# Kernel optimization log

Measured on AMD Instinct MI355X. Metric: run time of the kernel, lower is better.

Reference implementation:

```python
import jax, jax.numpy as jnp
import numpy as np
import math

B, S, D, H = 4, 2048, 1024, 16
DK = D // H


def setup_inputs() -> dict:
    key = jax.random.key(0)
    ks = jax.random.split(key, 11)
    s = 1.0 / math.sqrt(D)
    inp = {
        "query": jax.random.normal(ks[0], (B, S, D), jnp.float32),
        "key": jax.random.normal(ks[1], (B, S, D), jnp.float32),
        "value": jax.random.normal(ks[2], (B, S, D), jnp.float32),
        # torch nn.Linear params: weight [out,in], bias [out]
        "Wq": jax.random.uniform(ks[3], (D, D), jnp.float32, -s, s),
        "bq": jax.random.uniform(ks[4], (D,), jnp.float32, -s, s),
        "Wk": jax.random.uniform(ks[5], (D, D), jnp.float32, -s, s),
        "bk": jax.random.uniform(ks[6], (D,), jnp.float32, -s, s),
        "Wv": jax.random.uniform(ks[7], (D, D), jnp.float32, -s, s),
        "bv": jax.random.uniform(ks[8], (D,), jnp.float32, -s, s),
        "Wo": jax.random.uniform(ks[9], (D, D), jnp.float32, -s, s),
        "bo": jax.random.uniform(ks[10], (D,), jnp.float32, -s, s),
    }
    return inp


def _split_heads(x):
    # [B,S,D] -> [B,H,S,DK]
    return x.reshape(B, S, H, DK).transpose(0, 2, 1, 3)


def reference(query, key, value, Wq, bq, Wk, bk, Wv, bv, Wo, bo):
    q = _split_heads(query @ Wq.T + bq)
    k = _split_heads(key @ Wk.T + bk)
    v = _split_heads(value @ Wv.T + bv)
    scores = jnp.einsum("bhqd,bhkd->bhqk", q, k) / math.sqrt(DK)
    p = jax.nn.softmax(scores, axis=-1)  # dropout p=0 -> identity
    x = jnp.einsum("bhqk,bhkd->bhqd", p, v)
    x = x.transpose(0, 2, 1, 3).reshape(B, S, D)
    return x @ Wo.T + bo
```

## Files before the change

### kernel.cpp

```cpp
#include <hip/hip_runtime.h>
#include <hip/hip_bf16.h>


typedef __attribute__((ext_vector_type(8))) short bf16x8;
typedef __attribute__((ext_vector_type(4))) float f32x4;

static __device__ __forceinline__ unsigned short f2bf(float f) {
  union { __hip_bfloat16 h; unsigned short u; } cv;
  cv.h = __float2bfloat16(f);
  return cv.u;
}

static __device__ __forceinline__ unsigned int pack2bf(float a, float b) {
  union { __hip_bfloat162 h; unsigned int u; } cv;
  cv.h = __float22bfloat162_rn(float2{a, b});
  return cv.u;
}

static __device__ __forceinline__ void pl32swap(unsigned int& a, unsigned int& b) {
  asm volatile("v_permlane32_swap_b32 %0, %1" : "+v"(a), "+v"(b));
}
static __device__ __forceinline__ void pl16swap(unsigned int& a, unsigned int& b) {
  asm volatile("v_permlane16_swap_b32 %0, %1" : "+v"(a), "+v"(b));
}

static __device__ __forceinline__ void gload_lds16(const void* g, void* l) {
  __builtin_amdgcn_global_load_lds(
      (const __attribute__((address_space(1))) unsigned int*)g,
      (__attribute__((address_space(3))) unsigned int*)l, 16, 0, 0);
}

template<int NJ>
struct CvtJobs { const float* in[NJ]; unsigned short* out[NJ]; int n; };

template<int NJ>
__global__ __launch_bounds__(256) void cvt_batch(CvtJobs<NJ> jobs) {
  const float* __restrict__ in = jobs.in[blockIdx.y];
  unsigned short* __restrict__ out = jobs.out[blockIdx.y];
  int i = (blockIdx.x * 256 + threadIdx.x) * 4;
  if (i + 3 < jobs.n) {
    float4 v = *(const float4*)(in + i);
    ushort4 o;
    o.x = f2bf(v.x); o.y = f2bf(v.y); o.z = f2bf(v.z); o.w = f2bf(v.w);
    *(ushort4*)(out + i) = o;
  }
}

template<int MODE>
__global__ __launch_bounds__(256) void gemm_bt(const unsigned short* __restrict__ A_,
                                               const unsigned short* __restrict__ Bw_,
                                               const float* __restrict__ bias,
                                               const float* __restrict__ bias1,
                                               void* __restrict__ outp,
                                               int M, int N, int K) {
  __shared__ unsigned short As[128 * 32];
  __shared__ unsigned short Bs[128 * 32];
  const int tid = threadIdx.x;
  const int w = tid >> 6, lane = tid & 63;
  const int wr = w >> 1, wc = w & 1;
  const int fr = lane & 15, fg = lane >> 4;

  const unsigned short* A = A_;
  const unsigned short* Bw = Bw_;
  float scale = 1.f;
  unsigned short* out16 = (unsigned short*)outp;
  if (MODE == 4) {
    const int z = blockIdx.z;
    A += (size_t)z * (8192 * 1024);
    Bw += (size_t)z * (1024 * 1024);
    out16 += (size_t)z * (8192 * 1024);
    if (z == 0) scale = 0.18033688011f;
    else bias = bias1;
  }

  int bx, by;
  if (MODE != 2) {
    const int nwg = gridDim.x * gridDim.y;
    const int lin = blockIdx.y * gridDim.x + blockIdx.x;
    const int nb = (lin & 7) * (nwg >> 3) + (lin >> 3);
    bx = nb % gridDim.x; by = nb / gridDim.x;
  } else {
    bx = blockIdx.x; by = blockIdx.y;
  }
  const int m0 = by * 128, n0 = bx * 128;

  f32x4 acc[4][4] = {};
  const int e0 = (w * 2) * 512 + lane * 8;

  for (int kt = 0; kt < K; kt += 32) {
#pragma unroll
    for (int i = 0; i < 2; ++i) {
      const int e = e0 + i * 512;
      const int row = e >> 5, kk = e & 31;
      gload_lds16(A + (size_t)(m0 + row) * K + kt + kk, (void*)(As + e));
      gload_lds16(Bw + (size_t)(n0 + row) * K + kt + kk, (void*)(Bs + e));
    }
    __syncthreads();
    bf16x8 af[4], bfr[4];
#pragma unroll
    for (int m = 0; m < 4; ++m)
      af[m] = *(const bf16x8*)(As + (wr * 64 + m * 16 + fr) * 32 + fg * 8);
#pragma unroll
    for (int n = 0; n < 4; ++n)
      bfr[n] = *(const bf16x8*)(Bs + (wc * 64 + n * 16 + fr) * 32 + fg * 8);
#pragma unroll
    for (int m = 0; m < 4; ++m)
#pragma unroll
      for (int n = 0; n < 4; ++n)
        acc[m][n] = __builtin_amdgcn_mfma_f32_16x16x32_bf16(af[m], bfr[n], acc[m][n], 0, 0, 0);
    __syncthreads();
  }

#pragma unroll
  for (int m = 0; m < 4; ++m) {
#pragma unroll
    for (int n = 0; n < 4; ++n) {
      const int gn = n0 + wc * 64 + n * 16 + fr;
#pragma unroll
      for (int r = 0; r < 4; ++r) {
        const int gm = m0 + wr * 64 + m * 16 + fg * 4 + r;
        float val = acc[m][n][r];
        if (MODE == 2) val += bias[gm]; else val += bias[gn];
        if (MODE == 4) {
          val *= scale;
          size_t idx = ((size_t)((gm >> 11) * 16 + (gn >> 6)) * 2048 + (gm & 2047)) * 64 + (gn & 63);
          out16[idx] = f2bf(val);
        } else if (MODE == 2) {
          size_t idx = ((size_t)((gn >> 11) * 16 + (gm >> 6)) * 64 + (gm & 63)) * 2048 + (gn & 2047);
          out16[idx] = f2bf(val);
        } else {
          ((float*)outp)[(size_t)gm * N + gn] = val;
        }
      }
    }
  }
}

__global__ __launch_bounds__(256, 2) void attn_kernel(const unsigned short* __restrict__ Qh,
                                                      const unsigned short* __restrict__ Kh,
                                                      const unsigned short* __restrict__ Vt,
                                                      unsigned short* __restrict__ Xa) {
  const int S = 2048, DK = 64;
  const int tid = threadIdx.x;
  const int w = tid >> 6, lane = tid & 63;
  const int fr = lane & 15, fg = lane >> 4;

  const int bid = blockIdx.x;
  const int xcd = bid & 7, slot = bid >> 3;
  const int bh = xcd * 8 + (slot >> 3);
  const int qblk = slot & 7;
  const int q0 = qblk * 256 + w * 64;

  const unsigned short* Qp = Qh + (size_t)bh * S * DK;
  const unsigned short* Kp = Kh + (size_t)bh * S * DK;
  const unsigned short* Vp = Vt + (size_t)bh * DK * S;

  bf16x8 qf[4][2];
#pragma unroll
  for (int nt = 0; nt < 4; ++nt)
#pragma unroll
    for (int ks = 0; ks < 2; ++ks)
      qf[nt][ks] = *(const bf16x8*)(Qp + (size_t)(q0 + nt * 16 + fr) * DK + ks * 32 + fg * 8);

  bf16x8 ones;
#pragma unroll
  for (int j = 0; j < 8; ++j) ones[j] = (short)0x3F80;

  f32x4 xacc[4][4] = {};
  f32x4 xsum[4] = {};

  bf16x8 kf[4][2], vf[4][2];
#pragma unroll
  for (int mt = 0; mt < 4; ++mt)
#pragma unroll
    for (int ks = 0; ks < 2; ++ks)
      kf[mt][ks] = *(const bf16x8*)(Kp + (size_t)(mt * 16 + fr) * DK + ks * 32 + fg * 8);
#pragma unroll
  for (int dn = 0; dn < 4; ++dn)
#pragma unroll
    for (int ks = 0; ks < 2; ++ks)
      vf[dn][ks] = *(const bf16x8*)(Vp + (size_t)(dn * 16 + fr) * S + ks * 32 + fg * 8);

  for (int t = 0; t < 32; ++t) {
    const int kvn = ((t + 1) & 31) * 64;
#pragma unroll
    for (int nt = 0; nt < 4; ++nt) {
      f32x4 sc[4];
      __builtin_amdgcn_s_setprio(1);
#pragma unroll
      for (int mt = 0; mt < 4; ++mt) {
        sc[mt] = __builtin_amdgcn_mfma_f32_16x16x32_bf16(kf[mt][0], qf[nt][0],
                                                         (f32x4){0.f, 0.f, 0.f, 0.f}, 0, 0, 0);
        sc[mt] = __builtin_amdgcn_mfma_f32_16x16x32_bf16(kf[mt][1], qf[nt][1], sc[mt], 0, 0, 0);
      }
      __builtin_amdgcn_s_setprio(0);

      if (nt == 3) {
#pragma unroll
        for (int mt = 0; mt < 4; ++mt)
#pragma unroll
          for (int ks = 0; ks < 2; ++ks)
            kf[mt][ks] = *(const bf16x8*)(Kp + (size_t)(kvn + mt * 16 + fr) * DK + ks * 32 + fg * 8);
      }

      unsigned int X[4][2];
#pragma unroll
      for (int mt = 0; mt < 4; ++mt) {
        X[mt][0] = pack2bf(exp2f(sc[mt][0]), exp2f(sc[mt][1]));
        X[mt][1] = pack2bf(exp2f(sc[mt][2]), exp2f(sc[mt][3]));
      }

      union { unsigned int u[4]; bf16x8 v; } pa0, pa1;
      {
        unsigned int F0 = X[0][0], G0 = X[1][0]; pl32swap(F0, G0); pl16swap(F0, G0);
        unsigned int F1 = X[0][1], G1 = X[1][1]; pl32swap(F1, G1); pl16swap(F1, G1);
        pa0.u[0] = F0; pa0.u[1] = F1; pa0.u[2] = G0; pa0.u[3] = G1;
      }
      {
        unsigned int F0 = X[2][0], G0 = X[3][0]; pl32swap(F0, G0); pl16swap(F0, G0);
        unsigned int F1 = X[2][1], G1 = X[3][1]; pl32swap(F1, G1); pl16swap(F1, G1);
        pa1.u[0] = F0; pa1.u[1] = F1; pa1.u[2] = G0; pa1.u[3] = G1;
      }

      __builtin_amdgcn_s_setprio(1);
#pragma unroll
      for (int dn = 0; dn < 4; ++dn)
        xacc[nt][dn] = __builtin_amdgcn_mfma_f32_16x16x32_bf16(pa0.v, vf[dn][0], xacc[nt][dn], 0, 0, 0);
      xsum[nt] = __builtin_amdgcn_mfma_f32_16x16x32_bf16(pa0.v, ones, xsum[nt], 0, 0, 0);
      __builtin_amdgcn_s_setprio(0);
      if (nt == 3) {
#pragma unroll
        for (int dn = 0; dn < 4; ++dn)
          vf[dn][0] = *(const bf16x8*)(Vp + (size_t)(dn * 16 + fr) * S + kvn + fg * 8);
      }
      __builtin_amdgcn_s_setprio(1);
#pragma unroll
      for (int dn = 0; dn < 4; ++dn)
        xacc[nt][dn] = __builtin_amdgcn_mfma_f32_16x16x32_bf16(pa1.v, vf[dn][1], xacc[nt][dn], 0, 0, 0);
      xsum[nt] = __builtin_amdgcn_mfma_f32_16x16x32_bf16(pa1.v, ones, xsum[nt], 0, 0, 0);
      __builtin_amdgcn_s_setprio(0);
      if (nt == 3) {
#pragma unroll
        for (int dn = 0; dn < 4; ++dn)
          vf[dn][1] = *(const bf16x8*)(Vp + (size_t)(dn * 16 + fr) * S + kvn + 32 + fg * 8);
      }
    }
  }

  const int b = bh >> 4, h = bh & 15;
#pragma unroll
  for (int m = 0; m < 4; ++m) {
#pragma unroll
    for (int r = 0; r < 4; ++r) {
      const float inv = 1.f / xsum[m][r];
      const int s = q0 + m * 16 + fg * 4 + r;
      unsigned short* dst = Xa + ((size_t)(b * 2048 + s)) * 1024 + h * 64;
#pragma unroll
      for (int dn = 0; dn < 4; ++dn)
        dst[dn * 16 + fr] = f2bf(xacc[m][dn][r] * inv);
    }
  }
}

extern "C" void kernel_launch(void* const* d_in, const int* in_sizes, int n_in,
                              void* d_out, int out_size, void* d_ws, size_t ws_size,
                              hipStream_t stream) {
  (void)in_sizes; (void)n_in; (void)out_size;
  const float* q  = (const float*)d_in[0];
  const float* k  = (const float*)d_in[1];
  const float* v  = (const float*)d_in[2];
  const float* Wq = (const float*)d_in[3];
  const float* bq = (const float*)d_in[4];
  const float* Wk = (const float*)d_in[5];
  const float* bk = (const float*)d_in[6];
  const float* Wv = (const float*)d_in[7];
  const float* bv = (const float*)d_in[8];
  const float* Wo = (const float*)d_in[9];
  const float* bo = (const float*)d_in[10];
  float* out = (float*)d_out;

  const size_t XB = (size_t)8192 * 1024;
  const size_t WB = (size_t)1024 * 1024;
  const size_t need = (7 * XB + 4 * WB) * 2;
  if (ws_size < need) return;

  unsigned short* ws  = (unsigned short*)d_ws;
  unsigned short* xq  = ws;
  unsigned short* xk  = xq + XB;
  unsigned short* xv  = xk + XB;
  unsigned short* wqb = xv + XB;
  unsigned short* wkb = wqb + WB;
  unsigned short* wvb = wkb + WB;
  unsigned short* wob = wvb + WB;
  unsigned short* Qh  = wob + WB;
  unsigned short* Kh  = Qh + XB;
  unsigned short* Vt  = Kh + XB;
  unsigned short* Xa  = Vt + XB;

  CvtJobs<3> jx; jx.in[0] = q; jx.in[1] = k; jx.in[2] = v;
  jx.out[0] = xq; jx.out[1] = xk; jx.out[2] = xv; jx.n = (int)XB;
  cvt_batch<3><<<dim3(XB / 1024, 3), 256, 0, stream>>>(jx);
  CvtJobs<4> jw; jw.in[0] = Wq; jw.in[1] = Wk; jw.in[2] = Wv; jw.in[3] = Wo;
  jw.out[0] = wqb; jw.out[1] = wkb; jw.out[2] = wvb; jw.out[3] = wob; jw.n = (int)WB;
  cvt_batch<4><<<dim3(WB / 1024, 4), 256, 0, stream>>>(jw);

  gemm_bt<4><<<dim3(8, 64, 2), 256, 0, stream>>>(xq, wqb, bq, bk, Qh, 8192, 1024, 1024);
  gemm_bt<2><<<dim3(64, 8), 256, 0, stream>>>(wvb, xv, bv, nullptr, Vt, 1024, 8192, 1024);

  attn_kernel<<<dim3(512), 256, 0, stream>>>(Qh, Kh, Vt, Xa);

  gemm_bt<3><<<dim3(8, 64), 256, 0, stream>>>(Xa, wob, bo, nullptr, out, 8192, 1024, 1024);
}
```

Before: 399.1 us.

## Shrink attention tiles to 32 queries per wave and double grid for occupancy

The attention kernel now gives each wave 32 query rows instead of 64, steps K/V in 32-key chunks, and launches twice as many blocks with launch bounds raised to 4 blocks per CU. The explicit next-tile register prefetch of K and V is dropped; loads are now issued at the top of each chunk, and latency is meant to be hidden by more resident waves. The bf16 packing also switches to an inline v_cvt_pk_bf16_f32 instruction. The trade-off is that each K/V fragment is reused across fewer queries, so global and L2 traffic for K and V roughly doubles.

```diff
diff --git a/kernel.cpp b/kernel.cpp
--- a/kernel.cpp
+++ b/kernel.cpp
@@ -11,10 +11,10 @@
   return cv.u;
 }
 
-static __device__ __forceinline__ unsigned int pack2bf(float a, float b) {
-  union { __hip_bfloat162 h; unsigned int u; } cv;
-  cv.h = __float22bfloat162_rn(float2{a, b});
-  return cv.u;
+static __device__ __forceinline__ unsigned int cvtpk(float lo, float hi) {
+  unsigned int r;
+  asm("v_cvt_pk_bf16_f32 %0, %1, %2" : "=v"(r) : "v"(lo), "v"(hi));
+  return r;
 }
 
 static __device__ __forceinline__ void pl32swap(unsigned int& a, unsigned int& b) {
@@ -136,7 +136,7 @@
   }
 }
 
-__global__ __launch_bounds__(256, 2) void attn_kernel(const unsigned short* __restrict__ Qh,
+__global__ __launch_bounds__(256, 4) void attn_kernel(const unsigned short* __restrict__ Qh,
                                                       const unsigned short* __restrict__ Kh,
                                                       const unsigned short* __restrict__ Vt,
                                                       unsigned short* __restrict__ Xa) {
@@ -147,17 +147,17 @@
 
   const int bid = blockIdx.x;
   const int xcd = bid & 7, slot = bid >> 3;
-  const int bh = xcd * 8 + (slot >> 3);
-  const int qblk = slot & 7;
-  const int q0 = qblk * 256 + w * 64;
+  const int bh = xcd * 8 + (slot >> 4);
+  const int qblk = slot & 15;
+  const int q0 = qblk * 128 + w * 32;
 
   const unsigned short* Qp = Qh + (size_t)bh * S * DK;
   const unsigned short* Kp = Kh + (size_t)bh * S * DK;
   const unsigned short* Vp = Vt + (size_t)bh * DK * S;
 
-  bf16x8 qf[4][2];
-#pragma unroll
-  for (int nt = 0; nt < 4; ++nt)
+  bf16x8 qf[2][2];
+#pragma unroll
+  for (int nt = 0; nt < 2; ++nt)
 #pragma unroll
     for (int ks = 0; ks < 2; ++ks)
       qf[nt][ks] = *(const bf16x8*)(Qp + (size_t)(q0 + nt * 16 + fr) * DK + ks * 32 + fg * 8);
@@ -166,90 +166,54 @@
 #pragma unroll
   for (int j = 0; j < 8; ++j) ones[j] = (short)0x3F80;
 
-  f32x4 xacc[4][4] = {};
-  f32x4 xsum[4] = {};
-
-  bf16x8 kf[4][2], vf[4][2];
-#pragma unroll
-  for (int mt = 0; mt < 4; ++mt)
-#pragma unroll
-    for (int ks = 0; ks < 2; ++ks)
-      kf[mt][ks] = *(const bf16x8*)(Kp + (size_t)(mt * 16 + fr) * DK + ks * 32 + fg * 8);
-#pragma unroll
-  for (int dn = 0; dn < 4; ++dn)
-#pragma unroll
-    for (int ks = 0; ks < 2; ++ks)
-      vf[dn][ks] = *(const bf16x8*)(Vp + (size_t)(dn * 16 + fr) * S + ks * 32 + fg * 8);
-
-  for (int t = 0; t < 32; ++t) {
-    const int kvn = ((t + 1) & 31) * 64;
-#pragma unroll
-    for (int nt = 0; nt < 4; ++nt) {
-      f32x4 sc[4];
+  f32x4 xacc[2][4] = {};
+  f32x4 xsum[2] = {};
+
+  for (int kv2 = 0; kv2 < S; kv2 += 32) {
+    bf16x8 kh[2][2];
+#pragma unroll
+    for (int mt = 0; mt < 2; ++mt)
+#pragma unroll
+      for (int ks = 0; ks < 2; ++ks)
+        kh[mt][ks] = *(const bf16x8*)(Kp + (size_t)(kv2 + mt * 16 + fr) * DK + ks * 32 + fg * 8);
+    bf16x8 vk[4];
+#pragma unroll
+    for (int dn = 0; dn < 4; ++dn)
+      vk[dn] = *(const bf16x8*)(Vp + (size_t)(dn * 16 + fr) * S + kv2 + fg * 8);
+
+#pragma unroll
+    for (int nt = 0; nt < 2; ++nt) {
+      f32x4 s0, s1;
       __builtin_amdgcn_s_setprio(1);
-#pragma unroll
-      for (int mt = 0; mt < 4; ++mt) {
-        sc[mt] = __builtin_amdgcn_mfma_f32_16x16x32_bf16(kf[mt][0], qf[nt][0],
-                                                         (f32x4){0.f, 0.f, 0.f, 0.f}, 0, 0, 0);
-        sc[mt] = __builtin_amdgcn_mfma_f32_16x16x32_bf16(kf[mt][1], qf[nt][1], sc[mt], 0, 0, 0);
-      }
+      s0 = __builtin_amdgcn_mfma_f32_16x16x32_bf16(kh[0][0], qf[nt][0],
+                                                   (f32x4){0.f, 0.f, 0.f, 0.f}, 0, 0, 0);
+      s0 = __builtin_amdgcn_mfma_f32_16x16x32_bf16(kh[0][1], qf[nt][1], s0, 0, 0, 0);
+      s1 = __builtin_amdgcn_mfma_f32_16x16x32_bf16(kh[1][0], qf[nt][0],
+                                                   (f32x4){0.f, 0.f, 0.f, 0.f}, 0, 0, 0);
+      s1 = __builtin_amdgcn_mfma_f32_16x16x32_bf16(kh[1][1], qf[nt][1], s1, 0, 0, 0);
       __builtin_amdgcn_s_setprio(0);
 
-      if (nt == 3) {
-#pragma unroll
-        for (int mt = 0; mt < 4; ++mt)
-#pragma unroll
-          for (int ks = 0; ks < 2; ++ks)
-            kf[mt][ks] = *(const bf16x8*)(Kp + (size_t)(kvn + mt * 16 + fr) * DK + ks * 32 + fg * 8);
-      }
-
-      unsigned int X[4][2];
-#pragma unroll
-      for (int mt = 0; mt < 4; ++mt) {
-        X[mt][0] = pack2bf(exp2f(sc[mt][0]), exp2f(sc[mt][1]));
-        X[mt][1] = pack2bf(exp2f(sc[mt][2]), exp2f(sc[mt][3]));
-      }
-
-      union { unsigned int u[4]; bf16x8 v; } pa0, pa1;
-      {
-        unsigned int F0 = X[0][0], G0 = X[1][0]; pl32swap(F0, G0); pl16swap(F0, G0);
-        unsigned int F1 = X[0][1], G1 = X[1][1]; pl32swap(F1, G1); pl16swap(F1, G1);
-        pa0.u[0] = F0; pa0.u[1] = F1; pa0.u[2] = G0; pa0.u[3] = G1;
-      }
-      {
-        unsigned int F0 = X[2][0], G0 = X[3][0]; pl32swap(F0, G0); pl16swap(F0, G0);
-        unsigned int F1 = X[2][1], G1 = X[3][1]; pl32swap(F1, G1); pl16swap(F1, G1);
-        pa1.u[0] = F0; pa1.u[1] = F1; pa1.u[2] = G0; pa1.u[3] = G1;
-      }
+      unsigned int F0 = cvtpk(exp2f(s0[0]), exp2f(s0[1]));
+      unsigned int F1 = cvtpk(exp2f(s0[2]), exp2f(s0[3]));
+      unsigned int G0 = cvtpk(exp2f(s1[0]), exp2f(s1[1]));
+      unsigned int G1 = cvtpk(exp2f(s1[2]), exp2f(s1[3]));
+      pl32swap(F0, G0); pl16swap(F0, G0);
+      pl32swap(F1, G1); pl16swap(F1, G1);
+      union { unsigned int u[4]; bf16x8 v; } pa;
+      pa.u[0] = F0; pa.u[1] = F1; pa.u[2] = G0; pa.u[3] = G1;
 
       __builtin_amdgcn_s_setprio(1);
 #pragma unroll
       for (int dn = 0; dn < 4; ++dn)
-        xacc[nt][dn] = __builtin_amdgcn_mfma_f32_16x16x32_bf16(pa0.v, vf[dn][0], xacc[nt][dn], 0, 0, 0);
-      xsum[nt] = __builtin_amdgcn_mfma_f32_16x16x32_bf16(pa0.v, ones, xsum[nt], 0, 0, 0);
+        xacc[nt][dn] = __builtin_amdgcn_mfma_f32_16x16x32_bf16(pa.v, vk[dn], xacc[nt][dn], 0, 0, 0);
+      xsum[nt] = __builtin_amdgcn_mfma_f32_16x16x32_bf16(pa.v, ones, xsum[nt], 0, 0, 0);
       __builtin_amdgcn_s_setprio(0);
-      if (nt == 3) {
-#pragma unroll
-        for (int dn = 0; dn < 4; ++dn)
-          vf[dn][0] = *(const bf16x8*)(Vp + (size_t)(dn * 16 + fr) * S + kvn + fg * 8);
-      }
-      __builtin_amdgcn_s_setprio(1);
-#pragma unroll
-      for (int dn = 0; dn < 4; ++dn)
-        xacc[nt][dn] = __builtin_amdgcn_mfma_f32_16x16x32_bf16(pa1.v, vf[dn][1], xacc[nt][dn], 0, 0, 0);
-      xsum[nt] = __builtin_amdgcn_mfma_f32_16x16x32_bf16(pa1.v, ones, xsum[nt], 0, 0, 0);
-      __builtin_amdgcn_s_setprio(0);
-      if (nt == 3) {
-#pragma unroll
-        for (int dn = 0; dn < 4; ++dn)
-          vf[dn][1] = *(const bf16x8*)(Vp + (size_t)(dn * 16 + fr) * S + kvn + 32 + fg * 8);
-      }
     }
   }
 
   const int b = bh >> 4, h = bh & 15;
 #pragma unroll
-  for (int m = 0; m < 4; ++m) {
+  for (int m = 0; m < 2; ++m) {
 #pragma unroll
     for (int r = 0; r < 4; ++r) {
       const float inv = 1.f / xsum[m][r];
@@ -307,7 +271,7 @@
   gemm_bt<4><<<dim3(8, 64, 2), 256, 0, stream>>>(xq, wqb, bq, bk, Qh, 8192, 1024, 1024);
   gemm_bt<2><<<dim3(64, 8), 256, 0, stream>>>(wvb, xv, bv, nullptr, Vt, 1024, 8192, 1024);
 
-  attn_kernel<<<dim3(512), 256, 0, stream>>>(Qh, Kh, Vt, Xa);
+  attn_kernel<<<dim3(1024), 256, 0, stream>>>(Qh, Kh, Vt, Xa);
 
   gemm_bt<3><<<dim3(8, 64), 256, 0, stream>>>(Xa, wob, bo, nullptr, out, 8192, 1024, 1024);
 }
```

After: 502.6 us. +25.9%, slower.
